# Kernel tuning notes

Hardware: AMD Instinct MI355X
Metric: run time of the kernel (lower is better)

The kernel has to match this reference:

```python
import jax, jax.numpy as jnp
import numpy as np

H = 16
DH = 64  # n_state // n_head = 1024 // 16
EPS = 1e-6


def phi(x):
    return jax.nn.silu(x) + 1.0


def setup_inputs() -> dict:
    key = jax.random.key(0)
    ks = jax.random.split(key, 9)
    B, C, Tq, Tk = 8, 1024, 1500, 1500
    s = 1.0 / np.sqrt(C).astype(np.float32)
    return {
        "x": jax.random.normal(ks[0], (B, C, Tq, 1), jnp.float32),
        "xa": jax.random.normal(ks[1], (B, C, Tk, 1), jnp.float32),
        "Wq": jax.random.normal(ks[2], (C, C), jnp.float32) * s,
        "bq": jax.random.normal(ks[3], (C,), jnp.float32) * s,
        "Wk": jax.random.normal(ks[4], (C, C), jnp.float32) * s,
        "Wv": jax.random.normal(ks[5], (C, C), jnp.float32) * s,
        "bv": jax.random.normal(ks[6], (C,), jnp.float32) * s,
        "Wo": jax.random.normal(ks[7], (C, C), jnp.float32) * s,
        "bo": jax.random.normal(ks[8], (C,), jnp.float32) * s,
    }


def reference(x, xa, Wq, bq, Wk, Wv, bv, Wo, bo):
    # x: (B,C,Tq,1), xa: (B,C,Tk,1). 1x1 conv2d == matmul over channel dim.
    xq = x[..., 0]   # (B,C,Tq)
    xk = xa[..., 0]  # (B,C,Tk)
    q = jnp.einsum('oc,bct->bot', Wq, xq) + bq[None, :, None]
    k = jnp.einsum('oc,bct->bot', Wk, xk)  # key has no bias
    v = jnp.einsum('oc,bct->bot', Wv, xk) + bv[None, :, None]

    B, C, Tq = q.shape
    Tk = k.shape[2]
    pq = phi(q).reshape(B, H, DH, Tq)
    pk = phi(k).reshape(B, H, DH, Tk)
    vv = v.reshape(B, H, DH, Tk)

    k_sum = pk.sum(axis=3)            # (B,H,Dh) : sum_t phi(k)
    kv_sum = (pk * vv).sum(axis=3)    # (B,H,Dh) : diagonal phi(k)*v sum (as in source)
    den = jnp.einsum('bhdt,bhd->bht', pq, k_sum) + EPS  # (B,H,Tq)

    out = pq * kv_sum[..., None] / den[:, :, None, :]   # (B,H,Dh,Tq)
    out = out.reshape(B, C, Tq) / jnp.sqrt(jnp.asarray(DH, out.dtype))
    y = jnp.einsum('oc,bct->bot', Wo, out) + bo[None, :, None]
    return y[..., None]  # (B,C,Tq,1)
```

## Files before the change

### kernel.cpp

```cpp
#include <hip/hip_runtime.h>

typedef __attribute__((ext_vector_type(4))) float  f32x4;
typedef __attribute__((ext_vector_type(4))) float  float4v;
typedef __attribute__((ext_vector_type(8))) short  short8;
typedef __attribute__((ext_vector_type(4))) short  short4v;

#define TQ 1500
#define TP 1536
#define CC 1024
#define EPS 1e-6f

#define XT_OFF    ((size_t)0)
#define XAT_OFF   ((size_t)25165824)
#define OUT_OFF   ((size_t)50331648)
#define WB_OFF    ((size_t)75497472)
#define KSUM_OFF  ((size_t)83886080)
#define KVSUM_OFF ((size_t)83918848)

__device__ __forceinline__ float bf2f(short s) {
    union { unsigned u; float f; } v; v.u = ((unsigned)(unsigned short)s) << 16; return v.f;
}
__device__ __forceinline__ short f2bf(float f) {
    union { float f; unsigned u; } v; v.f = f;
    unsigned r = (v.u + 0x7FFFu + ((v.u >> 16) & 1u)) >> 16;
    return (short)r;
}
__device__ __forceinline__ float phi_f(float x) {
    return x / (1.f + __expf(-x)) + 1.f;
}
__device__ __forceinline__ void gl_lds16(const void* g, void* l) {
    __builtin_amdgcn_global_load_lds((const __attribute__((address_space(1))) void*)g,
                                     (__attribute__((address_space(3))) void*)l, 16, 0, 0);
}


__global__ __launch_bounds__(256)
void conv_w_kernel(const float* __restrict__ w0, const float* __restrict__ w1,
                   const float* __restrict__ w2, const float* __restrict__ w3,
                   short* __restrict__ o0, short* __restrict__ o1,
                   short* __restrict__ o2, short* __restrict__ o3)
{
    const int i = (blockIdx.x * 256 + threadIdx.x) * 4;
    float4v a = *(const float4v*)(w0 + i);
    float4v b = *(const float4v*)(w1 + i);
    float4v c = *(const float4v*)(w2 + i);
    float4v d = *(const float4v*)(w3 + i);
    short4v ra, rb, rc, rd;
#pragma unroll
    for (int j = 0; j < 4; ++j) {
        ra[j] = f2bf(a[j]); rb[j] = f2bf(b[j]); rc[j] = f2bf(c[j]); rd[j] = f2bf(d[j]);
    }
    *(short4v*)(o0 + i) = ra;
    *(short4v*)(o1 + i) = rb;
    *(short4v*)(o2 + i) = rc;
    *(short4v*)(o3 + i) = rd;
}

__global__ __launch_bounds__(256)
void xpose_kernel(const float* __restrict__ x, const float* __restrict__ xa,
                  short* __restrict__ xT, short* __restrict__ xaT)
{
    __shared__ float tile[64][65];
    const int z  = blockIdx.z;
    const int b  = z & 7;
    const float* src = (z < 8) ? x : xa;
    short* dst       = (z < 8) ? xT : xaT;
    const int c0 = blockIdx.y * 64;
    const int t0 = blockIdx.x * 64;
    const int tl = threadIdx.x & 63;
    const int q  = threadIdx.x >> 6;
    const int t  = t0 + tl;
#pragma unroll
    for (int i = 0; i < 16; ++i) {
        const int cl = q * 16 + i;
        float v = 0.f;
        if (t < TQ) v = src[((size_t)b * CC + c0 + cl) * TQ + t];
        tile[cl][tl] = v;
    }
    __syncthreads();
#pragma unroll
    for (int i = 0; i < 16; ++i) {
        const int t2 = q * 16 + i;
        dst[((size_t)b * TP + t0 + t2) * CC + c0 + tl] = f2bf(tile[tl][t2]);
    }
}

__global__ __launch_bounds__(256)
void gemm_kv_kernel(const short* __restrict__ xaT, const short* __restrict__ Wkb,
                    const short* __restrict__ Wvb, const float* __restrict__ bv,
                    float* __restrict__ ksum, float* __restrict__ kvsum)
{
    __shared__ short As[128 * 32];
    __shared__ short Bks[64 * 32];
    __shared__ short Bvs[64 * 32];
    const int f  = blockIdx.x;
    const int L  = (f & 7) * 192 + (f >> 3);
    const int nt = L % 16;
    const int mt = (L / 16) % 12;
    const int b  = L / 192;
    const int tid  = threadIdx.x;
    const int wave = tid >> 6, lane = tid & 63;
    const int wr = wave >> 1, wc = wave & 1;
    const int srow = lane >> 2;
    const int skof = (((lane & 3) ^ ((srow >> 1) & 3)) << 3);
    const int rl   = lane & 15;
    const int rg   = ((((lane >> 4)) ^ ((rl >> 1) & 3)) << 3);
    const int rgrp = lane >> 4;

    const short* Ab  = xaT + (size_t)b * TP * CC + (size_t)mt * 128 * CC;
    const short* Bkb = Wkb + (size_t)nt * 64 * CC;
    const short* Bvb = Wvb + (size_t)nt * 64 * CC;

    f32x4 ak[4][2] = {};
    f32x4 av[4][2] = {};

    for (int kt = 0; kt < CC / 32; ++kt) {
        const int k0 = kt << 5;
#pragma unroll
        for (int c2 = 0; c2 < 2; ++c2) {
            const int ch = wave * 2 + c2;
            gl_lds16(Ab + (size_t)(ch * 16 + srow) * CC + k0 + skof, &As[ch * 512]);
        }
        gl_lds16(Bkb + (size_t)(wave * 16 + srow) * CC + k0 + skof, &Bks[wave * 512]);
        gl_lds16(Bvb + (size_t)(wave * 16 + srow) * CC + k0 + skof, &Bvs[wave * 512]);
        __syncthreads();
        short8 ra[4], rk[2], rv[2];
#pragma unroll
        for (int i = 0; i < 4; ++i)
            ra[i] = *(const short8*)&As[(wr * 64 + i * 16 + rl) * 32 + rg];
#pragma unroll
        for (int j = 0; j < 2; ++j) {
            rk[j] = *(const short8*)&Bks[(wc * 32 + j * 16 + rl) * 32 + rg];
            rv[j] = *(const short8*)&Bvs[(wc * 32 + j * 16 + rl) * 32 + rg];
        }
#pragma unroll
        for (int i = 0; i < 4; ++i)
#pragma unroll
            for (int j = 0; j < 2; ++j) {
                ak[i][j] = __builtin_amdgcn_mfma_f32_16x16x32_bf16(ra[i], rk[j], ak[i][j], 0, 0, 0);
                av[i][j] = __builtin_amdgcn_mfma_f32_16x16x32_bf16(ra[i], rv[j], av[i][j], 0, 0, 0);
            }
        __syncthreads();
    }

#pragma unroll
    for (int j = 0; j < 2; ++j) {
        const int c = nt * 64 + wc * 32 + j * 16 + rl;
        const float bvc = bv[c];
        float sk = 0.f, skv = 0.f;
#pragma unroll
        for (int i = 0; i < 4; ++i) {
            const int tbase = mt * 128 + wr * 64 + i * 16 + rgrp * 4;
#pragma unroll
            for (int r = 0; r < 4; ++r) {
                if (tbase + r < TQ) {
                    float pk = phi_f(ak[i][j][r]);
                    float vv = av[i][j][r] + bvc;
                    sk  += pk;
                    skv += pk * vv;
                }
            }
        }
        sk  += __shfl_xor(sk, 16);  sk  += __shfl_xor(sk, 32);
        skv += __shfl_xor(skv, 16); skv += __shfl_xor(skv, 32);
        if (rgrp == 0) {
            atomicAdd(&ksum[b * CC + c], sk);
            atomicAdd(&kvsum[b * CC + c], skv);
        }
    }
}

__global__ __launch_bounds__(256)
void gemm_q_out_kernel(const short* __restrict__ xT, const short* __restrict__ Wqb,
                       const float* __restrict__ bq, const float* __restrict__ ksum,
                       const float* __restrict__ kvsum, short* __restrict__ outT)
{
    __shared__ short As[128 * 32];
    __shared__ short Bs[128 * 32];
    const int f  = blockIdx.x;
    const int L  = (f & 7) * 96 + (f >> 3);
    const int nt = L % 8;
    const int mt = (L / 8) % 12;
    const int b  = L / 96;
    const int tid  = threadIdx.x;
    const int wave = tid >> 6, lane = tid & 63;
    const int wr = wave >> 1, wc = wave & 1;
    const int srow = lane >> 2;
    const int skof = (((lane & 3) ^ ((srow >> 1) & 3)) << 3);
    const int rl   = lane & 15;
    const int rg   = ((((lane >> 4)) ^ ((rl >> 1) & 3)) << 3);
    const int rgrp = lane >> 4;

    const short* Ab = xT + (size_t)b * TP * CC + (size_t)mt * 128 * CC;
    const short* Bb = Wqb + (size_t)nt * 128 * CC;

    f32x4 acc[4][4] = {};

    for (int kt = 0; kt < CC / 32; ++kt) {
        const int k0 = kt << 5;
#pragma unroll
        for (int c2 = 0; c2 < 2; ++c2) {
            const int ch = wave * 2 + c2;
            gl_lds16(Ab + (size_t)(ch * 16 + srow) * CC + k0 + skof, &As[ch * 512]);
            gl_lds16(Bb + (size_t)(ch * 16 + srow) * CC + k0 + skof, &Bs[ch * 512]);
        }
        __syncthreads();
        short8 ra[4], rb[4];
#pragma unroll
        for (int i = 0; i < 4; ++i) {
            ra[i] = *(const short8*)&As[(wr * 64 + i * 16 + rl) * 32 + rg];
            rb[i] = *(const short8*)&Bs[(wc * 64 + i * 16 + rl) * 32 + rg];
        }
#pragma unroll
        for (int i = 0; i < 4; ++i)
#pragma unroll
            for (int j = 0; j < 4; ++j)
                acc[i][j] = __builtin_amdgcn_mfma_f32_16x16x32_bf16(ra[i], rb[j], acc[i][j], 0, 0, 0);
        __syncthreads();
    }

    float bias[4], ks[4], kv[4];
#pragma unroll
    for (int j = 0; j < 4; ++j) {
        const int c = nt * 128 + wc * 64 + j * 16 + rl;
        bias[j] = bq[c];
        ks[j]   = ksum[b * CC + c];
        kv[j]   = kvsum[b * CC + c];
    }
#pragma unroll
    for (int i = 0; i < 4; ++i)
#pragma unroll
        for (int j = 0; j < 4; ++j)
#pragma unroll
            for (int r = 0; r < 4; ++r)
                acc[i][j][r] = phi_f(acc[i][j][r] + bias[j]);
#pragma unroll
    for (int i = 0; i < 4; ++i) {
#pragma unroll
        for (int r = 0; r < 4; ++r) {
            float d = acc[i][0][r] * ks[0] + acc[i][1][r] * ks[1]
                    + acc[i][2][r] * ks[2] + acc[i][3][r] * ks[3];
            d += __shfl_xor(d, 1); d += __shfl_xor(d, 2);
            d += __shfl_xor(d, 4); d += __shfl_xor(d, 8);
            const float inv = 0.125f / (d + EPS);
            const int t = mt * 128 + wr * 64 + i * 16 + rgrp * 4 + r;
#pragma unroll
            for (int j = 0; j < 4; ++j) {
                const int c = nt * 128 + wc * 64 + j * 16 + rl;
                outT[((size_t)b * TP + t) * CC + c] = f2bf(acc[i][j][r] * kv[j] * inv);
            }
        }
    }
}

__global__ __launch_bounds__(256)
void gemm_o_kernel(const short* __restrict__ Wob, const short* __restrict__ outT,
                   const float* __restrict__ bo, float* __restrict__ y)
{
    __shared__ short As[128 * 32];
    __shared__ short Bs[128 * 32];
    const int f  = blockIdx.x;
    const int L  = (f & 7) * 96 + (f >> 3);
    const int tt = L % 12;
    const int ct = (L / 12) % 8;
    const int b  = L / 96;
    const int tid  = threadIdx.x;
    const int wave = tid >> 6, lane = tid & 63;
    const int wr = wave >> 1, wc = wave & 1;
    const int srow = lane >> 2;
    const int skof = (((lane & 3) ^ ((srow >> 1) & 3)) << 3);
    const int rl   = lane & 15;
    const int rg   = ((((lane >> 4)) ^ ((rl >> 1) & 3)) << 3);
    const int rgrp = lane >> 4;

    const short* Ab = Wob + (size_t)ct * 128 * CC;
    const short* Bb = outT + (size_t)b * TP * CC + (size_t)tt * 128 * CC;

    f32x4 acc[4][4] = {};

    for (int kt = 0; kt < CC / 32; ++kt) {
        const int k0 = kt << 5;
#pragma unroll
        for (int c2 = 0; c2 < 2; ++c2) {
            const int ch = wave * 2 + c2;
            gl_lds16(Ab + (size_t)(ch * 16 + srow) * CC + k0 + skof, &As[ch * 512]);
            gl_lds16(Bb + (size_t)(ch * 16 + srow) * CC + k0 + skof, &Bs[ch * 512]);
        }
        __syncthreads();
        short8 ra[4], rb[4];
#pragma unroll
        for (int i = 0; i < 4; ++i) {
            ra[i] = *(const short8*)&As[(wr * 64 + i * 16 + rl) * 32 + rg];
            rb[i] = *(const short8*)&Bs[(wc * 64 + i * 16 + rl) * 32 + rg];
        }
#pragma unroll
        for (int i = 0; i < 4; ++i)
#pragma unroll
            for (int j = 0; j < 4; ++j)
                acc[i][j] = __builtin_amdgcn_mfma_f32_16x16x32_bf16(ra[i], rb[j], acc[i][j], 0, 0, 0);
        __syncthreads();
    }

#pragma unroll
    for (int j = 0; j < 4; ++j) {
        const int tcol = tt * 128 + wc * 64 + j * 16 + rl;
        if (tcol >= TQ) continue;
#pragma unroll
        for (int i = 0; i < 4; ++i) {
            const int cbase = ct * 128 + wr * 64 + i * 16 + rgrp * 4;
#pragma unroll
            for (int r = 0; r < 4; ++r) {
                const int c = cbase + r;
                y[((size_t)b * CC + c) * TQ + tcol] = acc[i][j][r] + bo[c];
            }
        }
    }
}

extern "C" void kernel_launch(void* const* d_in, const int* in_sizes, int n_in,
                              void* d_out, int out_size, void* d_ws, size_t ws_size,
                              hipStream_t stream)
{
    (void)in_sizes; (void)n_in; (void)out_size; (void)ws_size;
    const float* x  = (const float*)d_in[0];
    const float* xa = (const float*)d_in[1];
    const float* Wq = (const float*)d_in[2];
    const float* bq = (const float*)d_in[3];
    const float* Wk = (const float*)d_in[4];
    const float* Wv = (const float*)d_in[5];
    const float* bv = (const float*)d_in[6];
    const float* Wo = (const float*)d_in[7];
    const float* bo = (const float*)d_in[8];
    float* y = (float*)d_out;
    char* ws = (char*)d_ws;

    short* xT    = (short*)(ws + XT_OFF);
    short* xaT   = (short*)(ws + XAT_OFF);
    short* outT  = (short*)(ws + OUT_OFF);
    short* Wqb   = (short*)(ws + WB_OFF);
    short* Wkb   = Wqb + (size_t)CC * CC;
    short* Wvb   = Wkb + (size_t)CC * CC;
    short* Wob   = Wvb + (size_t)CC * CC;
    float* ksum  = (float*)(ws + KSUM_OFF);
    float* kvsum = (float*)(ws + KVSUM_OFF);

    conv_w_kernel<<<dim3(CC * CC / 4 / 256), 256, 0, stream>>>(Wq, Wk, Wv, Wo, Wqb, Wkb, Wvb, Wob);
    xpose_kernel<<<dim3(TP / 64, CC / 64, 16), 256, 0, stream>>>(x, xa, xT, xaT);
    hipMemsetAsync(ws + KSUM_OFF, 0, 65536, stream);

    gemm_kv_kernel<<<dim3(1536), 256, 0, stream>>>(xaT, Wkb, Wvb, bv, ksum, kvsum);
    gemm_q_out_kernel<<<dim3(768), 256, 0, stream>>>(xT, Wqb, bq, ksum, kvsum, outT);
    gemm_o_kernel<<<dim3(768), 256, 0, stream>>>(Wob, outT, bo, y);
}
```

Measured before the change: 358.7 us.

## Pipeline GEMM K-loop with 4-stage LDS ring and 512-thread blocks

```diff
diff --git a/kernel.cpp b/kernel.cpp
--- a/kernel.cpp
+++ b/kernel.cpp
@@ -16,6 +16,13 @@
 #define WB_OFF    ((size_t)75497472)
 #define KSUM_OFF  ((size_t)83886080)
 #define KVSUM_OFF ((size_t)83918848)
+
+#define VMCNT4() asm volatile("s_waitcnt vmcnt(4)" ::: "memory")
+#define VMCNT2() asm volatile("s_waitcnt vmcnt(2)" ::: "memory")
+#define VMCNT0() asm volatile("s_waitcnt vmcnt(0)" ::: "memory")
+#define LGKM0()  asm volatile("s_waitcnt lgkmcnt(0)" ::: "memory")
+#define SBAR()   __builtin_amdgcn_s_barrier()
+#define SCHED0() __builtin_amdgcn_sched_barrier(0)
 
 __device__ __forceinline__ float bf2f(short s) {
     union { unsigned u; float f; } v; v.u = ((unsigned)(unsigned short)s) << 16; return v.f;
@@ -85,138 +92,74 @@
     }
 }
 
-__global__ __launch_bounds__(256)
-void gemm_kv_kernel(const short* __restrict__ xaT, const short* __restrict__ Wkb,
-                    const short* __restrict__ Wvb, const float* __restrict__ bv,
-                    float* __restrict__ ksum, float* __restrict__ kvsum)
-{
-    __shared__ short As[128 * 32];
-    __shared__ short Bks[64 * 32];
-    __shared__ short Bvs[64 * 32];
-    const int f  = blockIdx.x;
-    const int L  = (f & 7) * 192 + (f >> 3);
-    const int nt = L % 16;
-    const int mt = (L / 16) % 12;
-    const int b  = L / 192;
-    const int tid  = threadIdx.x;
-    const int wave = tid >> 6, lane = tid & 63;
-    const int wr = wave >> 1, wc = wave & 1;
-    const int srow = lane >> 2;
-    const int skof = (((lane & 3) ^ ((srow >> 1) & 3)) << 3);
-    const int rl   = lane & 15;
-    const int rg   = ((((lane >> 4)) ^ ((rl >> 1) & 3)) << 3);
-    const int rgrp = lane >> 4;
-
-    const short* Ab  = xaT + (size_t)b * TP * CC + (size_t)mt * 128 * CC;
-    const short* Bkb = Wkb + (size_t)nt * 64 * CC;
-    const short* Bvb = Wvb + (size_t)nt * 64 * CC;
-
-    f32x4 ak[4][2] = {};
-    f32x4 av[4][2] = {};
-
-    for (int kt = 0; kt < CC / 32; ++kt) {
-        const int k0 = kt << 5;
-#pragma unroll
-        for (int c2 = 0; c2 < 2; ++c2) {
-            const int ch = wave * 2 + c2;
-            gl_lds16(Ab + (size_t)(ch * 16 + srow) * CC + k0 + skof, &As[ch * 512]);
-        }
-        gl_lds16(Bkb + (size_t)(wave * 16 + srow) * CC + k0 + skof, &Bks[wave * 512]);
-        gl_lds16(Bvb + (size_t)(wave * 16 + srow) * CC + k0 + skof, &Bvs[wave * 512]);
-        __syncthreads();
-        short8 ra[4], rk[2], rv[2];
-#pragma unroll
-        for (int i = 0; i < 4; ++i)
-            ra[i] = *(const short8*)&As[(wr * 64 + i * 16 + rl) * 32 + rg];
-#pragma unroll
-        for (int j = 0; j < 2; ++j) {
-            rk[j] = *(const short8*)&Bks[(wc * 32 + j * 16 + rl) * 32 + rg];
-            rv[j] = *(const short8*)&Bvs[(wc * 32 + j * 16 + rl) * 32 + rg];
-        }
-#pragma unroll
-        for (int i = 0; i < 4; ++i)
-#pragma unroll
-            for (int j = 0; j < 2; ++j) {
-                ak[i][j] = __builtin_amdgcn_mfma_f32_16x16x32_bf16(ra[i], rk[j], ak[i][j], 0, 0, 0);
-                av[i][j] = __builtin_amdgcn_mfma_f32_16x16x32_bf16(ra[i], rv[j], av[i][j], 0, 0, 0);
-            }
-        __syncthreads();
-    }
-
-#pragma unroll
-    for (int j = 0; j < 2; ++j) {
-        const int c = nt * 64 + wc * 32 + j * 16 + rl;
-        const float bvc = bv[c];
-        float sk = 0.f, skv = 0.f;
-#pragma unroll
-        for (int i = 0; i < 4; ++i) {
-            const int tbase = mt * 128 + wr * 64 + i * 16 + rgrp * 4;
-#pragma unroll
-            for (int r = 0; r < 4; ++r) {
-                if (tbase + r < TQ) {
-                    float pk = phi_f(ak[i][j][r]);
-                    float vv = av[i][j][r] + bvc;
-                    sk  += pk;
-                    skv += pk * vv;
-                }
-            }
-        }
-        sk  += __shfl_xor(sk, 16);  sk  += __shfl_xor(sk, 32);
-        skv += __shfl_xor(skv, 16); skv += __shfl_xor(skv, 32);
-        if (rgrp == 0) {
-            atomicAdd(&ksum[b * CC + c], sk);
-            atomicAdd(&kvsum[b * CC + c], skv);
-        }
-    }
-}
-
-__global__ __launch_bounds__(256)
+
+__global__ __launch_bounds__(512, 4)
 void gemm_q_out_kernel(const short* __restrict__ xT, const short* __restrict__ Wqb,
                        const float* __restrict__ bq, const float* __restrict__ ksum,
                        const float* __restrict__ kvsum, short* __restrict__ outT)
 {
-    __shared__ short As[128 * 32];
-    __shared__ short Bs[128 * 32];
-    const int f  = blockIdx.x;
-    const int L  = (f & 7) * 96 + (f >> 3);
-    const int nt = L % 8;
-    const int mt = (L / 8) % 12;
-    const int b  = L / 96;
+    __shared__ short lds[4][8192];
+    const int f    = blockIdx.x;
+    const int L    = (f & 7) * 96 + (f >> 3);
+    const int nt   = L % 8;
+    const int mrow = L / 8;
+    const int b    = mrow / 12;
     const int tid  = threadIdx.x;
     const int wave = tid >> 6, lane = tid & 63;
-    const int wr = wave >> 1, wc = wave & 1;
-    const int srow = lane >> 2;
-    const int skof = (((lane & 3) ^ ((srow >> 1) & 3)) << 3);
-    const int rl   = lane & 15;
-    const int rg   = ((((lane >> 4)) ^ ((rl >> 1) & 3)) << 3);
-    const int rgrp = lane >> 4;
-
-    const short* Ab = xT + (size_t)b * TP * CC + (size_t)mt * 128 * CC;
-    const short* Bb = Wqb + (size_t)nt * 128 * CC;
-
-    f32x4 acc[4][4] = {};
-
-    for (int kt = 0; kt < CC / 32; ++kt) {
-        const int k0 = kt << 5;
-#pragma unroll
-        for (int c2 = 0; c2 < 2; ++c2) {
-            const int ch = wave * 2 + c2;
-            gl_lds16(Ab + (size_t)(ch * 16 + srow) * CC + k0 + skof, &As[ch * 512]);
-            gl_lds16(Bb + (size_t)(ch * 16 + srow) * CC + k0 + skof, &Bs[ch * 512]);
-        }
-        __syncthreads();
-        short8 ra[4], rb[4];
-#pragma unroll
-        for (int i = 0; i < 4; ++i) {
-            ra[i] = *(const short8*)&As[(wr * 64 + i * 16 + rl) * 32 + rg];
-            rb[i] = *(const short8*)&Bs[(wc * 64 + i * 16 + rl) * 32 + rg];
-        }
-#pragma unroll
-        for (int i = 0; i < 4; ++i)
+    const int wr = wave >> 1;
+    const int wc = wave & 1;
+    const int rl = lane & 15;
+    const int q4 = lane >> 4;
+    const int rg = (q4 ^ ((rl >> 1) & 3)) << 3;
+    const int rgrp = q4;
+
+    const int srow = tid >> 2;
+    const int skc  = ((tid & 3) ^ ((srow >> 1) & 3)) << 3;
+    const short* aSrc = xT  + (size_t)(mrow * 128 + srow) * CC + skc;
+    const short* bSrc = Wqb + (size_t)(nt   * 128 + srow) * CC + skc;
+    const int dstOff = wave * 512;
+
+    const int aoff0 = (wr * 32 + rl) * 32 + rg;
+    const int boff0 = 4096 + (wc * 64 + rl) * 32 + rg;
+
+    f32x4 acc[2][4] = {};
+
+#pragma unroll
+    for (int k0 = 0; k0 < 3; ++k0) {
+        gl_lds16(aSrc + k0 * 32, &lds[k0][dstOff]);
+        gl_lds16(bSrc + k0 * 32, &lds[k0][4096 + dstOff]);
+    }
+    VMCNT4(); SBAR();
+
+#pragma unroll 1
+    for (int kt = 0; kt < 32; ++kt) {
+        if (kt < 29) {
+            const int pn = (kt + 3) & 3;
+            gl_lds16(aSrc + (kt + 3) * 32, &lds[pn][dstOff]);
+            gl_lds16(bSrc + (kt + 3) * 32, &lds[pn][4096 + dstOff]);
+        }
+        const int p = kt & 3;
+        const short* ba = &lds[p][aoff0];
+        const short* bb = &lds[p][boff0];
+        short8 ra[2], rb[4];
+        ra[0] = *(const short8*)(ba);
+        ra[1] = *(const short8*)(ba + 512);
+        rb[0] = *(const short8*)(bb);
+        rb[1] = *(const short8*)(bb + 512);
+        rb[2] = *(const short8*)(bb + 1024);
+        rb[3] = *(const short8*)(bb + 1536);
+        LGKM0(); SCHED0();
+        __builtin_amdgcn_s_setprio(1);
+#pragma unroll
+        for (int i = 0; i < 2; ++i)
 #pragma unroll
             for (int j = 0; j < 4; ++j)
                 acc[i][j] = __builtin_amdgcn_mfma_f32_16x16x32_bf16(ra[i], rb[j], acc[i][j], 0, 0, 0);
-        __syncthreads();
+        __builtin_amdgcn_s_setprio(0);
+        if (kt < 29)       { VMCNT4(); }
+        else if (kt == 29) { VMCNT2(); }
+        else if (kt == 30) { VMCNT0(); }
+        if (kt < 31) SBAR();
     }
 
     float bias[4], ks[4], kv[4];
@@ -228,14 +171,14 @@
         kv[j]   = kvsum[b * CC + c];
     }
 #pragma unroll
-    for (int i = 0; i < 4; ++i)
+    for (int i = 0; i < 2; ++i)
 #pragma unroll
         for (int j = 0; j < 4; ++j)
 #pragma unroll
             for (int r = 0; r < 4; ++r)
                 acc[i][j][r] = phi_f(acc[i][j][r] + bias[j]);
 #pragma unroll
-    for (int i = 0; i < 4; ++i) {
+    for (int i = 0; i < 2; ++i) {
 #pragma unroll
         for (int r = 0; r < 4; ++r) {
             float d = acc[i][0][r] * ks[0] + acc[i][1][r] * ks[1]
@@ -243,75 +186,194 @@
             d += __shfl_xor(d, 1); d += __shfl_xor(d, 2);
             d += __shfl_xor(d, 4); d += __shfl_xor(d, 8);
             const float inv = 0.125f / (d + EPS);
-            const int t = mt * 128 + wr * 64 + i * 16 + rgrp * 4 + r;
+            const int trow = mrow * 128 + wr * 32 + i * 16 + rgrp * 4 + r;
 #pragma unroll
             for (int j = 0; j < 4; ++j) {
                 const int c = nt * 128 + wc * 64 + j * 16 + rl;
-                outT[((size_t)b * TP + t) * CC + c] = f2bf(acc[i][j][r] * kv[j] * inv);
+                outT[(size_t)trow * CC + c] = f2bf(acc[i][j][r] * kv[j] * inv);
             }
         }
     }
 }
 
-__global__ __launch_bounds__(256)
+__global__ __launch_bounds__(512, 4)
+void gemm_kv_kernel(const short* __restrict__ xaT, const short* __restrict__ Wkb,
+                    const short* __restrict__ Wvb, const float* __restrict__ bv,
+                    float* __restrict__ ksum, float* __restrict__ kvsum)
+{
+    __shared__ short lds[4][8192];
+    const int f    = blockIdx.x;
+    const int L    = (f & 7) * 192 + (f >> 3);
+    const int cb   = L % 16;
+    const int mrow = L / 16;
+    const int b    = mrow / 12;
+    const int tid  = threadIdx.x;
+    const int wave = tid >> 6, lane = tid & 63;
+    const int wr = wave >> 1;
+    const int wc = wave & 1;
+    const int rl = lane & 15;
+    const int q4 = lane >> 4;
+    const int rg = (q4 ^ ((rl >> 1) & 3)) << 3;
+    const int rgrp = q4;
+
+    const int srow = tid >> 2;
+    const int skc  = ((tid & 3) ^ ((srow >> 1) & 3)) << 3;
+    const short* aSrc = xaT + (size_t)(mrow * 128 + srow) * CC + skc;
+    const short* bSrc = (srow < 64)
+        ? Wkb + (size_t)(cb * 64 + srow) * CC + skc
+        : Wvb + (size_t)(cb * 64 + srow - 64) * CC + skc;
+    const int dstOff = wave * 512;
+
+    const int aoff0 = (wr * 32 + rl) * 32 + rg;
+    const int boffK = 4096 + (wc * 32 + rl) * 32 + rg;
+    const int boffV = boffK + 2048;
+
+    f32x4 acc[2][4] = {};
+
+#pragma unroll
+    for (int k0 = 0; k0 < 3; ++k0) {
+        gl_lds16(aSrc + k0 * 32, &lds[k0][dstOff]);
+        gl_lds16(bSrc + k0 * 32, &lds[k0][4096 + dstOff]);
+    }
+    VMCNT4(); SBAR();
+
+#pragma unroll 1
+    for (int kt = 0; kt < 32; ++kt) {
+        if (kt < 29) {
+            const int pn = (kt + 3) & 3;
+            gl_lds16(aSrc + (kt + 3) * 32, &lds[pn][dstOff]);
+            gl_lds16(bSrc + (kt + 3) * 32, &lds[pn][4096 + dstOff]);
+        }
+        const int p = kt & 3;
+        const short* ba = &lds[p][aoff0];
+        short8 ra[2], rb[4];
+        ra[0] = *(const short8*)(ba);
+        ra[1] = *(const short8*)(ba + 512);
+        rb[0] = *(const short8*)(&lds[p][boffK]);
+        rb[1] = *(const short8*)(&lds[p][boffK + 512]);
+        rb[2] = *(const short8*)(&lds[p][boffV]);
+        rb[3] = *(const short8*)(&lds[p][boffV + 512]);
+        LGKM0(); SCHED0();
+        __builtin_amdgcn_s_setprio(1);
+#pragma unroll
+        for (int i = 0; i < 2; ++i)
+#pragma unroll
+            for (int j = 0; j < 4; ++j)
+                acc[i][j] = __builtin_amdgcn_mfma_f32_16x16x32_bf16(ra[i], rb[j], acc[i][j], 0, 0, 0);
+        __builtin_amdgcn_s_setprio(0);
+        if (kt < 29)       { VMCNT4(); }
+        else if (kt == 29) { VMCNT2(); }
+        else if (kt == 30) { VMCNT0(); }
+        if (kt < 31) SBAR();
+    }
+
+    const int tbase = (mrow % 12) * 128 + wr * 32 + rgrp * 4;
+#pragma unroll
+    for (int jj = 0; jj < 2; ++jj) {
+        const int c = cb * 64 + wc * 32 + jj * 16 + rl;
+        const float bvc = bv[c];
+        float sk = 0.f, skv = 0.f;
+#pragma unroll
+        for (int i = 0; i < 2; ++i) {
+#pragma unroll
+            for (int r = 0; r < 4; ++r) {
+                if (tbase + i * 16 + r < TQ) {
+                    float pk = phi_f(acc[i][jj][r]);
+                    float vv = acc[i][jj + 2][r] + bvc;
+                    sk  += pk;
+                    skv += pk * vv;
+                }
+            }
+        }
+        sk  += __shfl_xor(sk, 16);  sk  += __shfl_xor(sk, 32);
+        skv += __shfl_xor(skv, 16); skv += __shfl_xor(skv, 32);
+        if (rgrp == 0) {
+            atomicAdd(&ksum[b * CC + c], sk);
+            atomicAdd(&kvsum[b * CC + c], skv);
+        }
+    }
+}
+
+__global__ __launch_bounds__(512, 4)
 void gemm_o_kernel(const short* __restrict__ Wob, const short* __restrict__ outT,
                    const float* __restrict__ bo, float* __restrict__ y)
 {
-    __shared__ short As[128 * 32];
-    __shared__ short Bs[128 * 32];
-    const int f  = blockIdx.x;
-    const int L  = (f & 7) * 96 + (f >> 3);
-    const int tt = L % 12;
-    const int ct = (L / 12) % 8;
-    const int b  = L / 96;
+    __shared__ short lds[4][8192];
+    const int f    = blockIdx.x;
+    const int L    = (f & 7) * 96 + (f >> 3);
+    const int ct   = L % 8;
+    const int rest = L / 8;
+    const int b    = rest / 12;
+    const int tt   = rest % 12;
     const int tid  = threadIdx.x;
     const int wave = tid >> 6, lane = tid & 63;
-    const int wr = wave >> 1, wc = wave & 1;
-    const int srow = lane >> 2;
-    const int skof = (((lane & 3) ^ ((srow >> 1) & 3)) << 3);
-    const int rl   = lane & 15;
-    const int rg   = ((((lane >> 4)) ^ ((rl >> 1) & 3)) << 3);
-    const int rgrp = lane >> 4;
-
-    const short* Ab = Wob + (size_t)ct * 128 * CC;
-    const short* Bb = outT + (size_t)b * TP * CC + (size_t)tt * 128 * CC;
-
-    f32x4 acc[4][4] = {};
-
-    for (int kt = 0; kt < CC / 32; ++kt) {
-        const int k0 = kt << 5;
-#pragma unroll
-        for (int c2 = 0; c2 < 2; ++c2) {
-            const int ch = wave * 2 + c2;
-            gl_lds16(Ab + (size_t)(ch * 16 + srow) * CC + k0 + skof, &As[ch * 512]);
-            gl_lds16(Bb + (size_t)(ch * 16 + srow) * CC + k0 + skof, &Bs[ch * 512]);
-        }
-        __syncthreads();
-        short8 ra[4], rb[4];
-#pragma unroll
-        for (int i = 0; i < 4; ++i) {
-            ra[i] = *(const short8*)&As[(wr * 64 + i * 16 + rl) * 32 + rg];
-            rb[i] = *(const short8*)&Bs[(wc * 64 + i * 16 + rl) * 32 + rg];
-        }
-#pragma unroll
-        for (int i = 0; i < 4; ++i)
+    const int wr = wave >> 1;
+    const int wc = wave & 1;
+    const int rl = lane & 15;
+    const int q4 = lane >> 4;
+    const int rg = (q4 ^ ((rl >> 1) & 3)) << 3;
+    const int rgrp = q4;
+
+    const int srow = tid >> 2;
+    const int skc  = ((tid & 3) ^ ((srow >> 1) & 3)) << 3;
+    const short* aSrc = Wob  + (size_t)(ct * 128 + srow) * CC + skc;
+    const short* bSrc = outT + (size_t)(rest * 128 + srow) * CC + skc;
+    const int dstOff = wave * 512;
+
+    const int aoff0 = (wr * 32 + rl) * 32 + rg;
+    const int boff0 = 4096 + (wc * 64 + rl) * 32 + rg;
+
+    f32x4 acc[2][4] = {};
+
+#pragma unroll
+    for (int k0 = 0; k0 < 3; ++k0) {
+        gl_lds16(aSrc + k0 * 32, &lds[k0][dstOff]);
+        gl_lds16(bSrc + k0 * 32, &lds[k0][4096 + dstOff]);
+    }
+    VMCNT4(); SBAR();
+
+#pragma unroll 1
+    for (int kt = 0; kt < 32; ++kt) {
+        if (kt < 29) {
+            const int pn = (kt + 3) & 3;
+            gl_lds16(aSrc + (kt + 3) * 32, &lds[pn][dstOff]);
+            gl_lds16(bSrc + (kt + 3) * 32, &lds[pn][4096 + dstOff]);
+        }
+        const int p = kt & 3;
+        const short* ba = &lds[p][aoff0];
+        const short* bb = &lds[p][boff0];
+        short8 ra[2], rb[4];
+        ra[0] = *(const short8*)(ba);
+        ra[1] = *(const short8*)(ba + 512);
+        rb[0] = *(const short8*)(bb);
+        rb[1] = *(const short8*)(bb + 512);
+        rb[2] = *(const short8*)(bb + 1024);
+        rb[3] = *(const short8*)(bb + 1536);
+        LGKM0(); SCHED0();
+        __builtin_amdgcn_s_setprio(1);
+#pragma unroll
+        for (int i = 0; i < 2; ++i)
 #pragma unroll
             for (int j = 0; j < 4; ++j)
                 acc[i][j] = __builtin_amdgcn_mfma_f32_16x16x32_bf16(ra[i], rb[j], acc[i][j], 0, 0, 0);
-        __syncthreads();
+        __builtin_amdgcn_s_setprio(0);
+        if (kt < 29)       { VMCNT4(); }
+        else if (kt == 29) { VMCNT2(); }
+        else if (kt == 30) { VMCNT0(); }
+        if (kt < 31) SBAR();
     }
 
 #pragma unroll
     for (int j = 0; j < 4; ++j) {
-        const int tcol = tt * 128 + wc * 64 + j * 16 + rl;
-        if (tcol >= TQ) continue;
-#pragma unroll
-        for (int i = 0; i < 4; ++i) {
-            const int cbase = ct * 128 + wr * 64 + i * 16 + rgrp * 4;
+        const int t = tt * 128 + wc * 64 + j * 16 + rl;
+        if (t >= TQ) continue;
+#pragma unroll
+        for (int i = 0; i < 2; ++i) {
+            const int cbase = ct * 128 + wr * 32 + i * 16 + rgrp * 4;
 #pragma unroll
             for (int r = 0; r < 4; ++r) {
                 const int c = cbase + r;
-                y[((size_t)b * CC + c) * TQ + tcol] = acc[i][j][r] + bo[c];
+                y[((size_t)b * CC + c) * TQ + t] = acc[i][j][r] + bo[c];
             }
         }
     }
@@ -348,7 +410,7 @@
     xpose_kernel<<<dim3(TP / 64, CC / 64, 16), 256, 0, stream>>>(x, xa, xT, xaT);
     hipMemsetAsync(ws + KSUM_OFF, 0, 65536, stream);
 
-    gemm_kv_kernel<<<dim3(1536), 256, 0, stream>>>(xaT, Wkb, Wvb, bv, ksum, kvsum);
-    gemm_q_out_kernel<<<dim3(768), 256, 0, stream>>>(xT, Wqb, bq, ksum, kvsum, outT);
-    gemm_o_kernel<<<dim3(768), 256, 0, stream>>>(Wob, outT, bo, y);
-}
+    gemm_kv_kernel<<<dim3(1536), 512, 0, stream>>>(xaT, Wkb, Wvb, bv, ksum, kvsum);
+    gemm_q_out_kernel<<<dim3(768), 512, 0, stream>>>(xT, Wqb, bq, ksum, kvsum, outT);
+    gemm_o_kernel<<<dim3(768), 512, 0, stream>>>(Wob, outT, bo, y);
+}
```

Measured after the change: 321.3 us. 10.4% less time.
